# Kernel tuning notes

Measured on AMD Instinct MI355X. Metric: run time of the kernel, lower is better.

The kernel has to match this reference:

```python
import jax, jax.numpy as jnp
import numpy as np

N_NODES = 100000
N_EDGES = 1600000
IN_DIM = 33
HID = 128
N_CLASSES = 10
N_GRAPHS = 128


def _glorot(key, shape):
    fan_in, fan_out = shape[0], shape[1]
    lim = (6.0 / (fan_in + fan_out)) ** 0.5
    return jax.random.uniform(key, shape, jnp.float32, -lim, lim)


def setup_inputs() -> dict:
    key = jax.random.key(0)
    ks = jax.random.split(key, 20)
    x = jax.random.normal(ks[0], (N_NODES, IN_DIM), jnp.float32)
    edge_index = jax.random.randint(ks[1], (2, N_EDGES), 0, N_NODES, jnp.int64)
    edge_w = jax.random.uniform(ks[2], (N_EDGES,), jnp.float32)
    batch = jnp.sort(jax.random.randint(ks[3], (N_NODES,), 0, N_GRAPHS, jnp.int64))
    p = {
        "We": _glorot(ks[4], (IN_DIM, HID)), "be": jnp.zeros((HID,), jnp.float32),
        "W1": _glorot(ks[5], (HID, HID)), "b1": jnp.zeros((HID,), jnp.float32),
        "W2": _glorot(ks[6], (HID, HID)), "b2": jnp.zeros((HID,), jnp.float32),
        "W3": _glorot(ks[7], (HID, HID)), "b3": jnp.zeros((HID,), jnp.float32),
        "W4": _glorot(ks[8], (HID, HID)), "b4": jnp.zeros((HID,), jnp.float32),
        "Wr1": _glorot(ks[9], (HID, HID // 2)), "br1": jnp.zeros((HID // 2,), jnp.float32),
        "Wr2": _glorot(ks[10], (HID // 2, HID // 4)), "br2": jnp.zeros((HID // 4,), jnp.float32),
        "Wr3": _glorot(ks[11], (HID // 4, N_CLASSES)),
    }
    return dict(x=x, edge_index=edge_index, edge_w=edge_w, batch=batch, **p)


def reference(x, edge_index, edge_w, batch,
              We, be, W1, b1, W2, b2, W3, b3, W4, b4,
              Wr1, br1, Wr2, br2, Wr3):
    N = x.shape[0]
    row, col = edge_index[0], edge_index[1]
    # PyG gcn_norm with add_self_loops=True: append (i,i) edges with weight 1
    loop = jnp.arange(N)
    row2 = jnp.concatenate([row, loop])
    col2 = jnp.concatenate([col, loop])
    w2 = jnp.concatenate([edge_w, jnp.ones((N,), edge_w.dtype)])
    deg = jax.ops.segment_sum(w2, col2, num_segments=N)  # in-degree incl. self-loop
    dinv = jnp.where(deg > 0, deg ** -0.5, 0.0)
    norm = dinv[row2] * w2 * dinv[col2]  # [E+N] symmetric normalization

    def conv(h, W, b):
        h = h @ W  # linear transform first (PyG GCNConv)
        msg = norm[:, None] * h[row2]  # gather + scale
        return jax.ops.segment_sum(msg, col2, num_segments=N) + b  # scatter-add to targets

    h = x @ We + be
    h = jax.nn.relu(conv(h, W1, b1))
    h = jax.nn.relu(conv(h, W2, b2))
    h = jax.nn.relu(conv(h, W3, b3))
    h = jax.nn.relu(conv(h, W4, b4))

    # global mean pool over graphs
    sums = jax.ops.segment_sum(h, batch, num_segments=N_GRAPHS)
    cnt = jax.ops.segment_sum(jnp.ones((N,), h.dtype), batch, num_segments=N_GRAPHS)
    pooled = sums / jnp.maximum(cnt, 1.0)[:, None]  # [G, HID]

    r = jax.nn.relu(pooled @ Wr1 + br1)
    r = jax.nn.relu(r @ Wr2 + br2)
    return r @ Wr3  # [G, n_classes]
```

## Files before the change

kernel.cpp:

```cpp
#include <hip/hip_runtime.h>
#include <hip/hip_bf16.h>

#define NN 100000
#define NE 1600000
#define IN_DIM 33
#define HID 128
#define NG 128
#define NCLS 10

using short8 = __attribute__((ext_vector_type(8))) short;
using floatx4 = __attribute__((ext_vector_type(4))) float;

static __device__ __forceinline__ size_t szmul(int a, int b) {
    return (size_t)a * (size_t)b;
}

static __device__ __forceinline__ unsigned short f2bf(float f) {
    unsigned u = __float_as_uint(f);
    u += 0x7fffu + ((u >> 16) & 1u);
    return (unsigned short)(u >> 16);
}
static __device__ __forceinline__ float bf_lo(unsigned u) { return __uint_as_float(u << 16); }
static __device__ __forceinline__ float bf_hi(unsigned u) { return __uint_as_float(u & 0xffff0000u); }

__global__ void k_init(int* bucket_cnt, int* bucket_fill, float* gsum) {
    int i = blockIdx.x * blockDim.x + threadIdx.x;
    if (i < 513) { bucket_cnt[i] = 0; bucket_fill[i] = 0; }
    if (i < NG * HID) gsum[i] = 0.0f;
}


__global__ __launch_bounds__(256) void k_bhist(const int* __restrict__ col,
                                               int* __restrict__ bucket_cnt, int e, int nbk) {
    __shared__ int hist[512];
    int tid = threadIdx.x;
    for (int i = tid; i < nbk; i += 256) hist[i] = 0;
    __syncthreads();
    for (int i = blockIdx.x * 256 + tid; i < e; i += 256 * 256)
        atomicAdd(&hist[col[i] >> 8], 1);
    __syncthreads();
    for (int i = tid; i < nbk; i += 256)
        if (hist[i]) atomicAdd(&bucket_cnt[i], hist[i]);
}

__global__ void k_scan_small(int* data, int nb) {
    __shared__ int s[512];
    int t = threadIdx.x;
    int v = (t < nb) ? data[t] : 0;
    s[t] = v;
    __syncthreads();
    for (int o = 1; o < 512; o <<= 1) {
        int a = (t >= o) ? s[t - o] : 0;
        __syncthreads();
        s[t] += a;
        __syncthreads();
    }
    if (t < nb) data[t] = s[t] - v;
    if (t == nb - 1) data[nb] = s[t];
}

__global__ __launch_bounds__(256) void k_bin_scatter(const int* __restrict__ row,
                                                     const int* __restrict__ col,
                                                     const float* __restrict__ w,
                                                     const int* __restrict__ bucket_base,
                                                     int* __restrict__ bucket_fill,
                                                     uint2* __restrict__ binned, int e, int nbk) {
    __shared__ int hist[512], rnk[512], basub[512];
    int tid = threadIdx.x;
    int c0 = blockIdx.x * 4096;
    for (int i = tid; i < nbk; i += 256) { hist[i] = 0; rnk[i] = 0; }
    __syncthreads();
    int base = c0 + tid * 16;
    int myb[16]; unsigned myp[16]; unsigned myw[16];
    if (base + 16 <= e) {
#pragma unroll
        for (int q = 0; q < 4; ++q) {
            int4 c4 = reinterpret_cast<const int4*>(col + base)[q];
            int4 r4 = reinterpret_cast<const int4*>(row + base)[q];
            float4 w4 = reinterpret_cast<const float4*>(w + base)[q];
            int cs[4] = {c4.x, c4.y, c4.z, c4.w};
            int rs[4] = {r4.x, r4.y, r4.z, r4.w};
            float ws[4] = {w4.x, w4.y, w4.z, w4.w};
#pragma unroll
            for (int v = 0; v < 4; ++v) {
                int c = cs[v];
                int b = c >> 8;
                myb[q * 4 + v] = b;
                myp[q * 4 + v] = ((unsigned)(c & 255) << 17) | (unsigned)rs[v];
                myw[q * 4 + v] = __float_as_uint(ws[v]);
                atomicAdd(&hist[b], 1);
            }
        }
    } else {
#pragma unroll
        for (int v = 0; v < 16; ++v) {
            int idx = base + v;
            int b = -1;
            if (idx < e) {
                int c = col[idx];
                myw[v] = __float_as_uint(w[idx]);
                b = c >> 8;
                myp[v] = ((unsigned)(c & 255) << 17) | (unsigned)row[idx];
                atomicAdd(&hist[b], 1);
            }
            myb[v] = b;
        }
    }
    __syncthreads();
    for (int i = tid; i < nbk; i += 256) {
        int c = hist[i];
        basub[i] = (c > 0) ? (bucket_base[i] + atomicAdd(&bucket_fill[i], c)) : 0;
    }
    __syncthreads();
#pragma unroll
    for (int u = 0; u < 16; ++u) {
        int b = myb[u];
        if (b >= 0) {
            int rk = atomicAdd(&rnk[b], 1);
            binned[basub[b] + rk] = make_uint2(myp[u], myw[u]);
        }
    }
}

__global__ __launch_bounds__(256) void k_bucket_rowptr(const uint2* __restrict__ binned,
                                                       const int* __restrict__ bucket_base,
                                                       int* __restrict__ rowptr,
                                                       float* __restrict__ wsum, int n) {
    __shared__ int c256[256];
    __shared__ float s256[256];
    __shared__ int sc[256];
    int b = blockIdx.x, tid = threadIdx.x;
    c256[tid] = 0;
    s256[tid] = 0.0f;
    __syncthreads();
    int beg = bucket_base[b], end = bucket_base[b + 1];
    for (int e2 = beg + tid; e2 < end; e2 += 256) {
        uint2 rec = binned[e2];
        int lo = (rec.x >> 17) & 255;
        atomicAdd(&c256[lo], 1);
        atomicAdd(&s256[lo], __uint_as_float(rec.y));
    }
    __syncthreads();
    int v = c256[tid];
    sc[tid] = v;
    __syncthreads();
    for (int o = 1; o < 256; o <<= 1) {
        int a = (tid >= o) ? sc[tid - o] : 0;
        __syncthreads();
        sc[tid] += a;
        __syncthreads();
    }
    int node = b * 256 + tid;
    if (node < n) {
        rowptr[node] = beg + sc[tid] - v;
        wsum[node] = s256[tid];
    }
}

__global__ void k_dinv(float* __restrict__ dinv, float* __restrict__ selfn,
                       int* __restrict__ rowptr, int n, int etot) {
    int i = blockIdx.x * blockDim.x + threadIdx.x;
    if (i == n) rowptr[n] = etot;
    if (i >= n) return;
    float d = 1.0f + dinv[i];
    float di = (d > 0.0f) ? (1.0f / sqrtf(d)) : 0.0f;
    dinv[i] = di;
    selfn[i] = di * di;
}

__global__ __launch_bounds__(256) void k_bucket_scatter(const uint2* __restrict__ binned,
                                                        const int* __restrict__ bucket_base,
                                                        const int* __restrict__ rowptr,
                                                        const float* __restrict__ dinv,
                                                        int2* __restrict__ csr, int n) {
    __shared__ int f256[256];
    int b = blockIdx.x, tid = threadIdx.x;
    f256[tid] = 0;
    __syncthreads();
    int beg = bucket_base[b], end = bucket_base[b + 1];
    for (int e2 = beg + tid; e2 < end; e2 += 256) {
        uint2 rec = binned[e2];
        int lo = (rec.x >> 17) & 255;
        int node = (b << 8) | lo;
        int src = rec.x & 0x1FFFF;
        float nw = dinv[src] * __uint_as_float(rec.y) * dinv[node];
        int pos = rowptr[node] + atomicAdd(&f256[lo], 1);
        csr[pos] = make_int2(src, __float_as_int(nw));
    }
    (void)n;
}

__global__ void k_combine(const float* __restrict__ We, const float* __restrict__ W1,
                          const float* __restrict__ be,
                          float* __restrict__ M, float* __restrict__ v) {
    int f = threadIdx.x;
    int k = blockIdx.x;
    if (k < IN_DIM) {
        float a = 0.0f;
#pragma unroll 8
        for (int j = 0; j < HID; ++j) a += We[k * HID + j] * W1[j * HID + f];
        M[k * HID + f] = a;
    } else {
        float a = 0.0f;
#pragma unroll 8
        for (int j = 0; j < HID; ++j) a += be[j] * W1[j * HID + f];
        v[f] = a;
    }
}

__global__ void k_wcast3(const float* __restrict__ W1, const float* __restrict__ W2,
                         const float* __restrict__ W3, unsigned short* __restrict__ Wt) {
    int k = blockIdx.x, c = threadIdx.x, l = blockIdx.y;
    const float* W = (l == 0) ? W1 : (l == 1) ? W2 : W3;
    Wt[((size_t)l * HID + c) * HID + k] = f2bf(W[k * HID + c]);
}

__global__ __launch_bounds__(256) void k_gemm_x(const float* __restrict__ x,
                                                const float* __restrict__ M,
                                                const float* __restrict__ v,
                                                unsigned short* __restrict__ tb, int n) {
    __shared__ float sX[32 * IN_DIM];
    int n0 = blockIdx.x * 32;
    int tid = threadIdx.x;
    int cnt = n - n0; if (cnt > 32) cnt = 32;
    for (int idx = tid; idx < cnt * IN_DIM; idx += 256)
        sX[idx] = x[szmul(n0, IN_DIM) + idx];
    __syncthreads();
    int f = tid & 127, g = tid >> 7;
    float Mc[IN_DIM];
#pragma unroll
    for (int k = 0; k < IN_DIM; ++k) Mc[k] = M[k * HID + f];
    float vf = v[f];
    int ndEnd = g * 16 + 16; if (ndEnd > cnt) ndEnd = cnt;
    for (int nd = g * 16; nd < ndEnd; ++nd) {
        float a = vf;
#pragma unroll
        for (int k = 0; k < IN_DIM; ++k) a += sX[nd * IN_DIM + k] * Mc[k];
        tb[szmul(n0 + nd, HID) + f] = f2bf(a);
    }
}

__global__ __launch_bounds__(256) void k_gemm_mfma(const unsigned short* __restrict__ A,
                                                   const unsigned short* __restrict__ Wt,
                                                   unsigned short* __restrict__ T, int n) {
    int wave = threadIdx.x >> 6;
    int lane = threadIdx.x & 63;
    int r = lane & 15, kg = lane >> 4;
    int row0 = blockIdx.x * 128 + wave * 32;
    short8 af0[4], af1[4];
#pragma unroll
    for (int kk = 0; kk < 4; ++kk) {
        int a0 = row0 + r, a1 = row0 + 16 + r;
        af0[kk] = (a0 < n) ? *reinterpret_cast<const short8*>(A + szmul(a0, HID) + kk * 32 + kg * 8)
                           : short8{0, 0, 0, 0, 0, 0, 0, 0};
        af1[kk] = (a1 < n) ? *reinterpret_cast<const short8*>(A + szmul(a1, HID) + kk * 32 + kg * 8)
                           : short8{0, 0, 0, 0, 0, 0, 0, 0};
    }
    floatx4 acc0[8], acc1[8];
#pragma unroll
    for (int ct = 0; ct < 8; ++ct) {
        acc0[ct] = floatx4{0.f, 0.f, 0.f, 0.f};
        acc1[ct] = floatx4{0.f, 0.f, 0.f, 0.f};
    }
#pragma unroll
    for (int kk = 0; kk < 4; ++kk) {
#pragma unroll
        for (int ct = 0; ct < 8; ++ct) {
            short8 bf = *reinterpret_cast<const short8*>(
                Wt + (size_t)(ct * 16 + r) * HID + kk * 32 + kg * 8);
            acc0[ct] = __builtin_amdgcn_mfma_f32_16x16x32_bf16(af0[kk], bf, acc0[ct], 0, 0, 0);
            acc1[ct] = __builtin_amdgcn_mfma_f32_16x16x32_bf16(af1[kk], bf, acc1[ct], 0, 0, 0);
        }
    }
    bool even = (r & 1) == 0;
#pragma unroll
    for (int ct = 0; ct < 8; ++ct) {
#pragma unroll
        for (int reg = 0; reg < 4; ++reg) {
            float o0 = __shfl_xor(acc0[ct][reg], 1);
            float o1 = __shfl_xor(acc1[ct][reg], 1);
            int orow0 = row0 + kg * 4 + reg;
            int orow1 = orow0 + 16;
            if (even && orow0 < n) {
                unsigned pk = (unsigned)f2bf(acc0[ct][reg]) | ((unsigned)f2bf(o0) << 16);
                *reinterpret_cast<unsigned*>(T + szmul(orow0, HID) + ct * 16 + r) = pk;
            }
            if (even && orow1 < n) {
                unsigned pk = (unsigned)f2bf(acc1[ct][reg]) | ((unsigned)f2bf(o1) << 16);
                *reinterpret_cast<unsigned*>(T + szmul(orow1, HID) + ct * 16 + r) = pk;
            }
        }
    }
}

__global__ __launch_bounds__(256) void k_aggregate(const uint4* __restrict__ tb,
                                                   const int* __restrict__ rowptr,
                                                   const int2* __restrict__ csr,
                                                   const float* __restrict__ selfn,
                                                   const float* __restrict__ bias,
                                                   uint4* __restrict__ hout, int n) {
    int i = (blockIdx.x * 256 + threadIdx.x) >> 4;
    if (i >= n) return;
    int p = threadIdx.x & 15;
    uint4 sv = tb[szmul(i, 16) + p];
    float sn = selfn[i];
    const float4* bp = reinterpret_cast<const float4*>(bias + p * 8);
    float4 b0 = bp[0], b1 = bp[1];
    float a0 = b0.x + sn * bf_lo(sv.x), a1 = b0.y + sn * bf_hi(sv.x);
    float a2 = b0.z + sn * bf_lo(sv.y), a3 = b0.w + sn * bf_hi(sv.y);
    float a4 = b1.x + sn * bf_lo(sv.z), a5 = b1.y + sn * bf_hi(sv.z);
    float a6 = b1.z + sn * bf_lo(sv.w), a7 = b1.w + sn * bf_hi(sv.w);
    int beg = rowptr[i], end = rowptr[i + 1];
#pragma unroll 4
    for (int j = beg; j < end; ++j) {
        int2 e = csr[j];
        float wj = __int_as_float(e.y);
        uint4 r = tb[szmul(e.x, 16) + p];
        a0 += wj * bf_lo(r.x); a1 += wj * bf_hi(r.x);
        a2 += wj * bf_lo(r.y); a3 += wj * bf_hi(r.y);
        a4 += wj * bf_lo(r.z); a5 += wj * bf_hi(r.z);
        a6 += wj * bf_lo(r.w); a7 += wj * bf_hi(r.w);
    }
    unsigned u0 = (unsigned)f2bf(fmaxf(a0, 0.f)) | ((unsigned)f2bf(fmaxf(a1, 0.f)) << 16);
    unsigned u1 = (unsigned)f2bf(fmaxf(a2, 0.f)) | ((unsigned)f2bf(fmaxf(a3, 0.f)) << 16);
    unsigned u2 = (unsigned)f2bf(fmaxf(a4, 0.f)) | ((unsigned)f2bf(fmaxf(a5, 0.f)) << 16);
    unsigned u3 = (unsigned)f2bf(fmaxf(a6, 0.f)) | ((unsigned)f2bf(fmaxf(a7, 0.f)) << 16);
    hout[szmul(i, 16) + p] = make_uint4(u0, u1, u2, u3);
}

__global__ void k_gcount_bs(const int* __restrict__ batch, int* gcnt, int n) {
    int g = threadIdx.x;
    if (g >= NG) return;
    int lo = 0, hi = n;
    while (lo < hi) { int mid = (lo + hi) >> 1; if (batch[mid] < g) lo = mid + 1; else hi = mid; }
    int start = lo;
    lo = 0; hi = n;
    while (lo < hi) { int mid = (lo + hi) >> 1; if (batch[mid] < g + 1) lo = mid + 1; else hi = mid; }
    gcnt[g] = lo - start;
}

__global__ __launch_bounds__(128) void k_pool(const unsigned short* __restrict__ h,
                                              const int* __restrict__ batch,
                                              float* gsum, int n) {
    int f = threadIdx.x;
    int i0 = blockIdx.x * 32;
    int i1 = min(i0 + 32, n);
    if (i0 >= n) return;
    float acc = 0.0f;
    int cur = batch[i0];
    for (int i = i0; i < i1; ++i) {
        int g = batch[i];
        if (g != cur) { atomicAdd(&gsum[cur * HID + f], acc); acc = 0.0f; cur = g; }
        acc += __uint_as_float((unsigned)h[szmul(i, HID) + f] << 16);
    }
    atomicAdd(&gsum[cur * HID + f], acc);
}

__global__ __launch_bounds__(128) void k_mlp(const float* __restrict__ gsum,
                                             const int* __restrict__ gcnt,
                                             const float* __restrict__ Wr1, const float* __restrict__ br1,
                                             const float* __restrict__ Wr2, const float* __restrict__ br2,
                                             const float* __restrict__ Wr3,
                                             float* __restrict__ out) {
    int g = blockIdx.x;
    int t = threadIdx.x;
    __shared__ float p[HID];
    __shared__ float r1[64];
    __shared__ float r2[32];
    float c = fmaxf((float)gcnt[g], 1.0f);
    p[t] = gsum[g * HID + t] / c;
    __syncthreads();
    if (t < 64) {
        float a = br1[t];
#pragma unroll 8
        for (int k = 0; k < HID; ++k) a += p[k] * Wr1[k * 64 + t];
        r1[t] = fmaxf(a, 0.0f);
    }
    __syncthreads();
    if (t < 32) {
        float a = br2[t];
#pragma unroll 8
        for (int k = 0; k < 64; ++k) a += r1[k] * Wr2[k * 32 + t];
        r2[t] = fmaxf(a, 0.0f);
    }
    __syncthreads();
    if (t < NCLS) {
        float a = 0.0f;
#pragma unroll
        for (int k = 0; k < 32; ++k) a += r2[k] * Wr3[k * NCLS + t];
        out[g * NCLS + t] = a;
    }
}

extern "C" void kernel_launch(void* const* d_in, const int* in_sizes, int n_in,
                              void* d_out, int out_size, void* d_ws, size_t ws_size,
                              hipStream_t stream) {
    const float* x     = (const float*)d_in[0];
    const int*   ei    = (const int*)d_in[1];
    const float* ew    = (const float*)d_in[2];
    const int*   batch = (const int*)d_in[3];
    const float* We  = (const float*)d_in[4];
    const float* be  = (const float*)d_in[5];
    const float* Wl[4] = { (const float*)d_in[6], (const float*)d_in[8],
                           (const float*)d_in[10], (const float*)d_in[12] };
    const float* bl[4] = { (const float*)d_in[7], (const float*)d_in[9],
                           (const float*)d_in[11], (const float*)d_in[13] };
    const float* Wr1 = (const float*)d_in[14];
    const float* br1 = (const float*)d_in[15];
    const float* Wr2 = (const float*)d_in[16];
    const float* br2 = (const float*)d_in[17];
    const float* Wr3 = (const float*)d_in[18];
    float* out = (float*)d_out;

    const int N = in_sizes[3];
    const int E = in_sizes[2];
    const int* row = ei;
    const int* col = ei + E;
    const int nbk = (N + 255) >> 8;

    char* w = (char*)d_ws;
    size_t off = 0;
    auto alloc = [&](size_t bytes) -> void* {
        void* p = w + off;
        off = (off + bytes + 255) & ~(size_t)255;
        return p;
    };
    float* dinv       = (float*)alloc((size_t)N * 4);
    float* selfn      = (float*)alloc((size_t)N * 4);
    int*   rowptr     = (int*)  alloc((size_t)(N + 1) * 4);
    int*   bucket_cnt = (int*)  alloc(513 * 4);
    int*   bucket_fill= (int*)  alloc(513 * 4);
    int2*  csr        = (int2*) alloc((size_t)E * 8);
    unsigned short* h  = (unsigned short*)alloc((size_t)N * HID * 2);
    unsigned short* tb = (unsigned short*)alloc((size_t)N * HID * 2);
    unsigned short* Wt = (unsigned short*)alloc((size_t)3 * HID * HID * 2);
    float* M          = (float*)alloc((size_t)IN_DIM * HID * 4);
    float* vbe        = (float*)alloc((size_t)HID * 4);
    float* gsum       = (float*)alloc((size_t)NG * HID * 4);
    int*   gcnt       = (int*)  alloc((size_t)NG * 4);
    uint2* binned     = (uint2*)tb;
    (void)ws_size;

    auto cdiv = [](int a, int b) { return (a + b - 1) / b; };

    k_init<<<64, 256, 0, stream>>>(bucket_cnt, bucket_fill, gsum);
    k_bhist<<<256, 256, 0, stream>>>(col, bucket_cnt, E, nbk);
    k_scan_small<<<1, 512, 0, stream>>>(bucket_cnt, nbk);
    k_bin_scatter<<<cdiv(E, 4096), 256, 0, stream>>>(row, col, ew, bucket_cnt,
                                                     bucket_fill, binned, E, nbk);
    k_bucket_rowptr<<<nbk, 256, 0, stream>>>(binned, bucket_cnt, rowptr, dinv, N);
    k_dinv<<<cdiv(N + 1, 256), 256, 0, stream>>>(dinv, selfn, rowptr, N, E);
    k_bucket_scatter<<<nbk, 256, 0, stream>>>(binned, bucket_cnt, rowptr, dinv, csr, N);

    k_combine<<<IN_DIM + 1, HID, 0, stream>>>(We, Wl[0], be, M, vbe);
    k_wcast3<<<dim3(HID, 3), HID, 0, stream>>>(Wl[1], Wl[2], Wl[3], Wt);

    k_gemm_x<<<cdiv(N, 32), 256, 0, stream>>>(x, M, vbe, tb, N);
    k_aggregate<<<cdiv(N, 16), 256, 0, stream>>>((const uint4*)tb, rowptr, csr,
                                                 selfn, bl[0], (uint4*)h, N);

    for (int l = 1; l < 4; ++l) {
        k_gemm_mfma<<<cdiv(N, 128), 256, 0, stream>>>(h, Wt + (size_t)(l - 1) * HID * HID,
                                                      tb, N);
        k_aggregate<<<cdiv(N, 16), 256, 0, stream>>>((const uint4*)tb, rowptr, csr,
                                                     selfn, bl[l], (uint4*)h, N);
    }

    k_gcount_bs<<<1, 128, 0, stream>>>(batch, gcnt, N);
    k_pool<<<cdiv(N, 32), 128, 0, stream>>>(h, batch, gsum, N);
    k_mlp<<<NG, HID, 0, stream>>>(gsum, gcnt, Wr1, br1, Wr2, br2, Wr3, out);

    (void)out_size; (void)n_in;
}
```

Before: 470.1 us.

## Fuse neighbor aggregation with next-layer MFMA GEMM via shared-memory staging

Three of the aggregate kernels are merged with the following bf16 MFMA GEMM into one kernel. Each block aggregates 64 nodes into a swizzled LDS tile, then multiplies that tile by the next layer's weights and writes the transformed features. This avoids writing the intermediate hidden activations to global memory, reading them back, and paying for the extra launches. In exchange, the GEMM tile per block shrinks from 128 to 64 rows, and the irregular gather phase is serialized before the MFMA phase within each block.

```diff
diff --git a/kernel.cpp b/kernel.cpp
--- a/kernel.cpp
+++ b/kernel.cpp
@@ -240,54 +240,85 @@
     }
 }
 
-__global__ __launch_bounds__(256) void k_gemm_mfma(const unsigned short* __restrict__ A,
-                                                   const unsigned short* __restrict__ Wt,
-                                                   unsigned short* __restrict__ T, int n) {
-    int wave = threadIdx.x >> 6;
-    int lane = threadIdx.x & 63;
+__global__ __launch_bounds__(256) void k_agg_gemm(const uint4* __restrict__ tb,
+                                                  const int* __restrict__ rowptr,
+                                                  const int2* __restrict__ csr,
+                                                  const float* __restrict__ selfn,
+                                                  const float* __restrict__ bias,
+                                                  const unsigned short* __restrict__ Wt,
+                                                  unsigned short* __restrict__ Tout, int n) {
+    __shared__ unsigned short sh[64][HID];
+    int tid = threadIdx.x;
+    int grp = tid >> 4;
+    int p = tid & 15;
+    int nbase = blockIdx.x * 64;
+    const float4* bp = reinterpret_cast<const float4*>(bias + p * 8);
+    float4 b0 = bp[0], b1 = bp[1];
+#pragma unroll
+    for (int sub = 0; sub < 4; ++sub) {
+        int rrow = sub * 16 + grp;
+        int i = nbase + rrow;
+        unsigned u0 = 0, u1 = 0, u2 = 0, u3 = 0;
+        if (i < n) {
+            uint4 sv = tb[szmul(i, 16) + p];
+            float sn = selfn[i];
+            float a0 = b0.x + sn * bf_lo(sv.x), a1 = b0.y + sn * bf_hi(sv.x);
+            float a2 = b0.z + sn * bf_lo(sv.y), a3 = b0.w + sn * bf_hi(sv.y);
+            float a4 = b1.x + sn * bf_lo(sv.z), a5 = b1.y + sn * bf_hi(sv.z);
+            float a6 = b1.z + sn * bf_lo(sv.w), a7 = b1.w + sn * bf_hi(sv.w);
+            int beg = rowptr[i], end = rowptr[i + 1];
+#pragma unroll 4
+            for (int j = beg; j < end; ++j) {
+                int2 e = csr[j];
+                float wj = __int_as_float(e.y);
+                uint4 r = tb[szmul(e.x, 16) + p];
+                a0 += wj * bf_lo(r.x); a1 += wj * bf_hi(r.x);
+                a2 += wj * bf_lo(r.y); a3 += wj * bf_hi(r.y);
+                a4 += wj * bf_lo(r.z); a5 += wj * bf_hi(r.z);
+                a6 += wj * bf_lo(r.w); a7 += wj * bf_hi(r.w);
+            }
+            u0 = (unsigned)f2bf(fmaxf(a0, 0.f)) | ((unsigned)f2bf(fmaxf(a1, 0.f)) << 16);
+            u1 = (unsigned)f2bf(fmaxf(a2, 0.f)) | ((unsigned)f2bf(fmaxf(a3, 0.f)) << 16);
+            u2 = (unsigned)f2bf(fmaxf(a4, 0.f)) | ((unsigned)f2bf(fmaxf(a5, 0.f)) << 16);
+            u3 = (unsigned)f2bf(fmaxf(a6, 0.f)) | ((unsigned)f2bf(fmaxf(a7, 0.f)) << 16);
+        }
+        int chunk = p ^ (rrow & 7);
+        *reinterpret_cast<uint4*>(&sh[rrow][chunk * 8]) = make_uint4(u0, u1, u2, u3);
+    }
+    __syncthreads();
+    int wave = tid >> 6;
+    int lane = tid & 63;
     int r = lane & 15, kg = lane >> 4;
-    int row0 = blockIdx.x * 128 + wave * 32;
-    short8 af0[4], af1[4];
+    int rrow = wave * 16 + r;
+    short8 af[4];
 #pragma unroll
     for (int kk = 0; kk < 4; ++kk) {
-        int a0 = row0 + r, a1 = row0 + 16 + r;
-        af0[kk] = (a0 < n) ? *reinterpret_cast<const short8*>(A + szmul(a0, HID) + kk * 32 + kg * 8)
-                           : short8{0, 0, 0, 0, 0, 0, 0, 0};
-        af1[kk] = (a1 < n) ? *reinterpret_cast<const short8*>(A + szmul(a1, HID) + kk * 32 + kg * 8)
-                           : short8{0, 0, 0, 0, 0, 0, 0, 0};
-    }
-    floatx4 acc0[8], acc1[8];
-#pragma unroll
-    for (int ct = 0; ct < 8; ++ct) {
-        acc0[ct] = floatx4{0.f, 0.f, 0.f, 0.f};
-        acc1[ct] = floatx4{0.f, 0.f, 0.f, 0.f};
-    }
+        int chunk = (kk * 4 + kg) ^ (rrow & 7);
+        af[kk] = *reinterpret_cast<const short8*>(&sh[rrow][chunk * 8]);
+    }
+    floatx4 acc[8];
+#pragma unroll
+    for (int ct = 0; ct < 8; ++ct) acc[ct] = floatx4{0.f, 0.f, 0.f, 0.f};
 #pragma unroll
     for (int kk = 0; kk < 4; ++kk) {
 #pragma unroll
         for (int ct = 0; ct < 8; ++ct) {
             short8 bf = *reinterpret_cast<const short8*>(
                 Wt + (size_t)(ct * 16 + r) * HID + kk * 32 + kg * 8);
-            acc0[ct] = __builtin_amdgcn_mfma_f32_16x16x32_bf16(af0[kk], bf, acc0[ct], 0, 0, 0);
-            acc1[ct] = __builtin_amdgcn_mfma_f32_16x16x32_bf16(af1[kk], bf, acc1[ct], 0, 0, 0);
+            acc[ct] = __builtin_amdgcn_mfma_f32_16x16x32_bf16(af[kk], bf, acc[ct], 0, 0, 0);
         }
     }
     bool even = (r & 1) == 0;
+    int row0 = nbase + wave * 16;
 #pragma unroll
     for (int ct = 0; ct < 8; ++ct) {
 #pragma unroll
         for (int reg = 0; reg < 4; ++reg) {
-            float o0 = __shfl_xor(acc0[ct][reg], 1);
-            float o1 = __shfl_xor(acc1[ct][reg], 1);
-            int orow0 = row0 + kg * 4 + reg;
-            int orow1 = orow0 + 16;
-            if (even && orow0 < n) {
-                unsigned pk = (unsigned)f2bf(acc0[ct][reg]) | ((unsigned)f2bf(o0) << 16);
-                *reinterpret_cast<unsigned*>(T + szmul(orow0, HID) + ct * 16 + r) = pk;
-            }
-            if (even && orow1 < n) {
-                unsigned pk = (unsigned)f2bf(acc1[ct][reg]) | ((unsigned)f2bf(o1) << 16);
-                *reinterpret_cast<unsigned*>(T + szmul(orow1, HID) + ct * 16 + r) = pk;
+            float o = __shfl_xor(acc[ct][reg], 1);
+            int orow = row0 + kg * 4 + reg;
+            if (even && orow < n) {
+                unsigned pk = (unsigned)f2bf(acc[ct][reg]) | ((unsigned)f2bf(o) << 16);
+                *reinterpret_cast<unsigned*>(Tout + szmul(orow, HID) + ct * 16 + r) = pk;
             }
         }
     }
@@ -431,14 +462,15 @@
     int*   bucket_cnt = (int*)  alloc(513 * 4);
     int*   bucket_fill= (int*)  alloc(513 * 4);
     int2*  csr        = (int2*) alloc((size_t)E * 8);
-    unsigned short* h  = (unsigned short*)alloc((size_t)N * HID * 2);
-    unsigned short* tb = (unsigned short*)alloc((size_t)N * HID * 2);
+    unsigned short* bufA = (unsigned short*)alloc((size_t)N * HID * 2);
+    unsigned short* bufB = (unsigned short*)alloc((size_t)N * HID * 2);
+    unsigned short* hfin = (unsigned short*)alloc((size_t)N * HID * 2);
     unsigned short* Wt = (unsigned short*)alloc((size_t)3 * HID * HID * 2);
     float* M          = (float*)alloc((size_t)IN_DIM * HID * 4);
     float* vbe        = (float*)alloc((size_t)HID * 4);
     float* gsum       = (float*)alloc((size_t)NG * HID * 4);
     int*   gcnt       = (int*)  alloc((size_t)NG * 4);
-    uint2* binned     = (uint2*)tb;
+    uint2* binned     = (uint2*)bufA;
     (void)ws_size;
 
     auto cdiv = [](int a, int b) { return (a + b - 1) / b; };
@@ -455,19 +487,18 @@
     k_combine<<<IN_DIM + 1, HID, 0, stream>>>(We, Wl[0], be, M, vbe);
     k_wcast3<<<dim3(HID, 3), HID, 0, stream>>>(Wl[1], Wl[2], Wl[3], Wt);
 
-    k_gemm_x<<<cdiv(N, 32), 256, 0, stream>>>(x, M, vbe, tb, N);
-    k_aggregate<<<cdiv(N, 16), 256, 0, stream>>>((const uint4*)tb, rowptr, csr,
-                                                 selfn, bl[0], (uint4*)h, N);
-
-    for (int l = 1; l < 4; ++l) {
-        k_gemm_mfma<<<cdiv(N, 128), 256, 0, stream>>>(h, Wt + (size_t)(l - 1) * HID * HID,
-                                                      tb, N);
-        k_aggregate<<<cdiv(N, 16), 256, 0, stream>>>((const uint4*)tb, rowptr, csr,
-                                                     selfn, bl[l], (uint4*)h, N);
-    }
+    k_gemm_x<<<cdiv(N, 32), 256, 0, stream>>>(x, M, vbe, bufB, N);
+    k_agg_gemm<<<cdiv(N, 64), 256, 0, stream>>>((const uint4*)bufB, rowptr, csr, selfn,
+                                                bl[0], Wt + 0 * (size_t)HID * HID, bufA, N);
+    k_agg_gemm<<<cdiv(N, 64), 256, 0, stream>>>((const uint4*)bufA, rowptr, csr, selfn,
+                                                bl[1], Wt + 1 * (size_t)HID * HID, bufB, N);
+    k_agg_gemm<<<cdiv(N, 64), 256, 0, stream>>>((const uint4*)bufB, rowptr, csr, selfn,
+                                                bl[2], Wt + 2 * (size_t)HID * HID, bufA, N);
+    k_aggregate<<<cdiv(N, 16), 256, 0, stream>>>((const uint4*)bufA, rowptr, csr,
+                                                 selfn, bl[3], (uint4*)hfin, N);
 
     k_gcount_bs<<<1, 128, 0, stream>>>(batch, gcnt, N);
-    k_pool<<<cdiv(N, 32), 128, 0, stream>>>(h, batch, gsum, N);
+    k_pool<<<cdiv(N, 32), 128, 0, stream>>>(hfin, batch, gsum, N);
     k_mlp<<<NG, HID, 0, stream>>>(gsum, gcnt, Wr1, br1, Wr2, br2, Wr3, out);
 
     (void)out_size; (void)n_in;
```

After: 485.4 us. +3.3%, slower.
